# Optimization experiments

Hardware: AMD Instinct MI355X
Metric: run time of the kernel (lower is better)

The kernel has to match this reference:

```python
import jax, jax.numpy as jnp
import numpy as np

N = 50000          # num nodes
E = 1_600_000      # num edges (avg degree 32)
F = 512            # node_dim
C = 64             # num_clusters
O = 256            # output_dim


def setup_inputs() -> dict:
    key = jax.random.key(0)
    ks = jax.random.split(key, 9)
    lim_p = 1.0 / np.sqrt(F)
    inp = {
        "x": jax.random.normal(ks[0], (N, F), dtype=jnp.float32),
        "edge_index": jax.random.randint(ks[1], (2, E), 0, N, dtype=jnp.int64),
        "batch": jnp.zeros((N,), dtype=jnp.int64),
        # gnn_pool: Linear(F, C)
        "Wp": jax.random.uniform(ks[2], (F, C), jnp.float32, -lim_p, lim_p),
        "bp": jax.random.uniform(ks[3], (C,), jnp.float32, -lim_p, lim_p),
        # gnn_embed: Linear(F, F)
        "We": jax.random.uniform(ks[4], (F, F), jnp.float32, -lim_p, lim_p),
        "be": jax.random.uniform(ks[5], (F,), jnp.float32, -lim_p, lim_p),
        # projection: Linear(F, O)
        "Wo": jax.random.uniform(ks[6], (F, O), jnp.float32, -lim_p, lim_p),
        "bo": jax.random.uniform(ks[7], (O,), jnp.float32, -lim_p, lim_p),
    }
    return inp


def reference(x, edge_index, batch, Wp, bp, We, be, Wo, bo):
    # s = softmax(gnn_pool(x), -1): soft cluster assignments  [N, C]
    s = jax.nn.softmax(x @ Wp + bp, axis=-1)
    # h = gnn_embed(x)  [N, F]
    h = x @ We + be
    # dense_diff_pool pooled features: out = s^T h  -> [C, F]
    # (out_adj = s^T A s and the link/entropy reg are computed by the
    #  original but discarded; they do not affect the returned output.)
    pooled = jnp.einsum("nc,nf->cf", s, h)
    # PyG dense_diff_pool unsqueezes 2D inputs to batch dim 1 -> [1, C, F]
    out = pooled[None] @ Wo + bo  # [1, C, O]
    return out
```

## Files before the change

kernel.cpp:

```cpp
#include <hip/hip_runtime.h>
#include <hip/hip_bf16.h>

typedef __attribute__((ext_vector_type(8))) short short8;
typedef __attribute__((ext_vector_type(4))) float floatx4;
typedef __attribute__((ext_vector_type(4))) unsigned uint4v;

#define FDIM 512
#define CDIM 64
#define ODIM 256
#define XSS 520
#define STS 72
#define XSW(r, f) ((f) ^ ((((r) >> 3) & 3) << 4))

__device__ __forceinline__ ushort f2bf(float f) {
    union { float f; unsigned u; } v; v.f = f;
    unsigned r = v.u + 0x7FFFu + ((v.u >> 16) & 1u);
    return (ushort)(r >> 16);
}
__device__ __forceinline__ float bf2f(unsigned hi16) {
    union { unsigned u; float f; } v; v.u = hi16 << 16; return v.f;
}

__global__ __launch_bounds__(256) void kWpT(const float* __restrict__ Wp,
                                            ushort* __restrict__ WpT) {
    int g = blockIdx.x * 256 + threadIdx.x;
    int f = g >> 6, c = g & 63;
    WpT[c * FDIM + f] = f2bf(Wp[f * CDIM + c]);
}

__global__ __launch_bounds__(512, 2) void kFused(
        const float* __restrict__ x, const ushort* __restrict__ WpT,
        const float* __restrict__ bp, ushort* __restrict__ part,
        float* __restrict__ cpart, int N, int nTiles, int P) {
    __shared__ ushort xs[64][XSS];
    __shared__ ushort sT[64][STS];
    __shared__ float red1[64][4];
    __shared__ float red2[64][4];

    const int t    = threadIdx.x;
    const int w    = t >> 6;
    const int lane = t & 63;
    const int l16  = lane & 15;
    const int q    = lane >> 4;
    const int ci   = w & 3;
    const int rg   = w >> 2;

    floatx4 acc[4][4];
#pragma unroll
    for (int mt = 0; mt < 4; ++mt)
#pragma unroll
        for (int nt = 0; nt < 4; ++nt) acc[mt][nt] = (floatx4){0.f, 0.f, 0.f, 0.f};
    float csp[4] = {0.f, 0.f, 0.f, 0.f};

    float bpv[4];
#pragma unroll
    for (int reg = 0; reg < 4; ++reg) bpv[reg] = bp[16 * ci + 4 * q + reg];

    const ushort* wb = WpT + (size_t)(16 * ci + l16) * FDIM + q * 8;
    const int permA0 = (((l16 >> 3) & 1)) << 4;
    const int permA1 = ((2 + ((l16 >> 3) & 1)) & 3) << 4;

    for (int tile = blockIdx.x; tile < nTiles; tile += P) {
        __syncthreads();
        const int row0 = tile * 64;

#pragma unroll
        for (int half = 0; half < 2; ++half) {
            floatx4 vv[8];
#pragma unroll
            for (int j = 0; j < 8; ++j) {
                int v = (half * 8 + j) * 512 + t;
                int r = v >> 7;
                int f4 = (v & 127) << 2;
                vv[j] = (floatx4){0.f, 0.f, 0.f, 0.f};
                if (row0 + r < N)
                    vv[j] = *(const floatx4*)(x + (size_t)(row0 + r) * FDIM + f4);
            }
#pragma unroll
            for (int j = 0; j < 8; ++j) {
                int v = (half * 8 + j) * 512 + t;
                int r = v >> 7;
                int f4 = (v & 127) << 2;
                uint2 pk;
                pk.x = (unsigned)f2bf(vv[j][0]) | ((unsigned)f2bf(vv[j][1]) << 16);
                pk.y = (unsigned)f2bf(vv[j][2]) | ((unsigned)f2bf(vv[j][3]) << 16);
                *(uint2*)&xs[r][XSW(r, f4)] = pk;
            }
        }
        __syncthreads();

        floatx4 acc1[2];
        acc1[0] = (floatx4){0.f, 0.f, 0.f, 0.f};
        acc1[1] = (floatx4){0.f, 0.f, 0.f, 0.f};
        const int r0p = 16 * (2 * rg) + l16;
        const int r1p = 16 * (2 * rg + 1) + l16;
#pragma unroll
        for (int kb = 0; kb < 4; ++kb) {
            short8 af[4];
#pragma unroll
            for (int ki = 0; ki < 4; ++ki)
                af[ki] = *(const short8*)(wb + kb * 128 + ki * 32);
#pragma unroll
            for (int ki = 0; ki < 4; ++ki) {
                const int cb = kb * 128 + ki * 32 + q * 8;
                short8 b0 = *(const short8*)&xs[r0p][cb ^ permA0];
                acc1[0] = __builtin_amdgcn_mfma_f32_16x16x32_bf16(af[ki], b0, acc1[0], 0, 0, 0);
                short8 b1 = *(const short8*)&xs[r1p][cb ^ permA1];
                acc1[1] = __builtin_amdgcn_mfma_f32_16x16x32_bf16(af[ki], b1, acc1[1], 0, 0, 0);
            }
        }

        float lg[2][4], rmax[2], rsi[2];
#pragma unroll
        for (int rt = 0; rt < 2; ++rt) {
#pragma unroll
            for (int reg = 0; reg < 4; ++reg) lg[rt][reg] = acc1[rt][reg] + bpv[reg];
            float m = fmaxf(fmaxf(lg[rt][0], lg[rt][1]), fmaxf(lg[rt][2], lg[rt][3]));
            m = fmaxf(m, __shfl_xor(m, 16));
            m = fmaxf(m, __shfl_xor(m, 32));
            if (lane < 16) red1[16 * (2 * rg + rt) + lane][ci] = m;
        }
        __syncthreads();
#pragma unroll
        for (int rt = 0; rt < 2; ++rt) {
            const int row = 16 * (2 * rg + rt) + l16;
            rmax[rt] = fmaxf(fmaxf(red1[row][0], red1[row][1]),
                             fmaxf(red1[row][2], red1[row][3]));
        }
#pragma unroll
        for (int rt = 0; rt < 2; ++rt) {
            float p = 0.f;
#pragma unroll
            for (int reg = 0; reg < 4; ++reg) {
                float e = __expf(lg[rt][reg] - rmax[rt]);
                lg[rt][reg] = e; p += e;
            }
            p += __shfl_xor(p, 16);
            p += __shfl_xor(p, 32);
            if (lane < 16) red2[16 * (2 * rg + rt) + lane][ci] = p;
        }
        __syncthreads();
#pragma unroll
        for (int rt = 0; rt < 2; ++rt) {
            const int row = 16 * (2 * rg + rt) + l16;
            rsi[rt] = 1.0f / (red2[row][0] + red2[row][1] +
                              red2[row][2] + red2[row][3]);
        }
#pragma unroll
        for (int rt = 0; rt < 2; ++rt) {
            const int row = 16 * (2 * rg + rt) + l16;
            bool valid = (row0 + row) < N;
#pragma unroll
            for (int reg = 0; reg < 4; ++reg) {
                float s = valid ? lg[rt][reg] * rsi[rt] : 0.f;
                sT[16 * ci + 4 * q + reg][row] = f2bf(s);
                csp[reg] += s;
            }
        }
        __syncthreads();

        short8 as_[2][4];
#pragma unroll
        for (int ks = 0; ks < 2; ++ks)
#pragma unroll
            for (int mt = 0; mt < 4; ++mt)
                as_[ks][mt] = *(const short8*)&sT[16 * mt + l16][ks * 32 + q * 8];
#pragma unroll
        for (int nt = 0; nt < 4; ++nt) {
            const int fcol = (64 * w + 16 * nt + l16) ^ (q << 4);
            short8 b0, b1;
#pragma unroll
            for (int j = 0; j < 8; ++j) {
                b0[j] = (short)xs[q * 8 + j][fcol];
                b1[j] = (short)xs[32 + q * 8 + j][fcol];
            }
#pragma unroll
            for (int mt = 0; mt < 4; ++mt) {
                acc[mt][nt] = __builtin_amdgcn_mfma_f32_16x16x32_bf16(
                    as_[0][mt], b0, acc[mt][nt], 0, 0, 0);
                acc[mt][nt] = __builtin_amdgcn_mfma_f32_16x16x32_bf16(
                    as_[1][mt], b1, acc[mt][nt], 0, 0, 0);
            }
        }
    }

#pragma unroll
    for (int reg = 0; reg < 4; ++reg) {
        float v = csp[reg];
        v += __shfl_xor(v, 1); v += __shfl_xor(v, 2);
        v += __shfl_xor(v, 4); v += __shfl_xor(v, 8);
        if (l16 == 0) red1[16 * ci + 4 * q + reg][rg] = v;
    }
    __syncthreads();
    if (t < 64) cpart[(size_t)blockIdx.x * CDIM + t] = red1[t][0] + red1[t][1];

    ushort* xf = &xs[0][0];
#pragma unroll
    for (int mt = 0; mt < 4; ++mt)
#pragma unroll
        for (int nt = 0; nt < 4; ++nt)
#pragma unroll
            for (int reg = 0; reg < 4; ++reg)
                xf[(16 * mt + 4 * q + reg) * FDIM + 64 * w + 16 * nt + l16] =
                    f2bf(acc[mt][nt][reg]);
    __syncthreads();
    const uint4v* src = (const uint4v*)xf;
    uint4v* dst = (uint4v*)(part + (size_t)blockIdx.x * (CDIM * FDIM));
#pragma unroll
    for (int i = 0; i < 8; ++i)
        dst[i * 512 + t] = src[i * 512 + t];
}

__global__ __launch_bounds__(512) void kR(const ushort* __restrict__ part,
                                          const float* __restrict__ cpart,
                                          float* __restrict__ colsum,
                                          float* __restrict__ Mp,
                                          int P, int pch) {
    __shared__ float ws8[8];
    const int c = blockIdx.x, pc = blockIdx.y, t = threadIdx.x;
    const int p0 = pc * pch, p1 = min(p0 + pch, P);

    float sum = 0.f;
    const ushort* pp = part + (size_t)c * FDIM + t;
#pragma unroll 4
    for (int p = p0; p < p1; ++p)
        sum += bf2f((unsigned)pp[(size_t)p * (CDIM * FDIM)]);
    Mp[((size_t)pc * CDIM + c) * FDIM + t] = sum;

    float cv = 0.f;
    {
        int p = p0 + t;
        if (p < p1) cv = cpart[(size_t)p * CDIM + c];
    }
    cv += __shfl_xor(cv, 1);  cv += __shfl_xor(cv, 2);
    cv += __shfl_xor(cv, 4);  cv += __shfl_xor(cv, 8);
    cv += __shfl_xor(cv, 16); cv += __shfl_xor(cv, 32);
    if ((t & 63) == 0) ws8[t >> 6] = cv;
    __syncthreads();
    if (t == 0) {
        float tot = 0.f;
#pragma unroll
        for (int i = 0; i < 8; ++i) tot += ws8[i];
        atomicAdd(colsum + c, tot);
    }
}

__global__ __launch_bounds__(512) void kC(const float* __restrict__ Mp,
                                          const float* __restrict__ colsum,
                                          const float* __restrict__ We,
                                          const float* __restrict__ be,
                                          const float* __restrict__ Wo,
                                          const float* __restrict__ bo,
                                          float* __restrict__ out) {
    __shared__ float Mrow[512];
    __shared__ float pooled[512];
    __shared__ float halves[2][256];
    const int c = blockIdx.x, t = threadIdx.x;

    float sum = 0.f;
#pragma unroll
    for (int pc = 0; pc < 8; ++pc)
        sum += Mp[((size_t)pc * CDIM + c) * FDIM + t];
    Mrow[t] = sum;
    __syncthreads();

    float a = colsum[c] * be[t];
#pragma unroll 16
    for (int k = 0; k < FDIM; ++k)
        a = fmaf(Mrow[k], We[(size_t)k * FDIM + t], a);
    pooled[t] = a;
    __syncthreads();

    const int o = t & 255, h = t >> 8;
    float b = 0.f;
#pragma unroll 16
    for (int kk = 0; kk < 256; ++kk) {
        int k = h * 256 + kk;
        b = fmaf(pooled[k], Wo[(size_t)k * ODIM + o], b);
    }
    halves[h][o] = b;
    __syncthreads();
    if (t < 256)
        out[(size_t)c * ODIM + t] = halves[0][t] + halves[1][t] + bo[t];
}

extern "C" void kernel_launch(void* const* d_in, const int* in_sizes, int n_in,
                              void* d_out, int out_size, void* d_ws, size_t ws_size,
                              hipStream_t stream) {
    const float* x  = (const float*)d_in[0];
    const float* Wp = (const float*)d_in[3];
    const float* bp = (const float*)d_in[4];
    const float* We = (const float*)d_in[5];
    const float* be = (const float*)d_in[6];
    const float* Wo = (const float*)d_in[7];
    const float* bo = (const float*)d_in[8];
    float* out = (float*)d_out;

    const int N = in_sizes[0] / FDIM;
    const int nTiles = (N + 63) / 64;

    char*   wsb    = (char*)d_ws;
    ushort* WpT    = (ushort*)wsb;
    float*  colsum = (float*)(wsb + 65536);
    float*  cpart  = (float*)(wsb + 66560);
    float*  Mp     = (float*)(wsb + 266752);
    const size_t PART_OFF = 1315328;
    ushort* part   = (ushort*)(wsb + PART_OFF);

    size_t avail = (ws_size > PART_OFF + 65536) ? (ws_size - PART_OFF) / 65536 : 1;
    int P = (int)(avail < (size_t)nTiles ? avail : (size_t)nTiles);
    if (P < 1) P = 1;
    const int pch = (P + 7) / 8;

    hipMemsetAsync(colsum, 0, 256, stream);
    kWpT<<<128, 256, 0, stream>>>(Wp, WpT);
    kFused<<<P, 512, 0, stream>>>(x, WpT, bp, part, cpart, N, nTiles, P);
    kR<<<dim3(CDIM, 8), 512, 0, stream>>>(part, cpart, colsum, Mp, P, pch);
    kC<<<CDIM, 512, 0, stream>>>(Mp, colsum, We, be, Wo, bo, out);
}
```

Before: 257.6 us.

## Stream x tiles into LDS via global_load_lds, halve tile rows, cap grid

Changes the x staging from register loads plus bf16 conversion into swizzled LDS to direct global-to-LDS DMA of fp32 rows, with conversion to bf16 done at MFMA operand read time. The row tile shrinks from 64 to 32 so the fp32 tile fits, and occupancy is raised to 4 blocks per CU. The grid is capped at 512 persistent blocks rather than one per tile, which reduces partial-result traffic in the reduction stage. In exchange, each tile pays extra per-element conversion work in both GEMMs, does more loop iterations with their barriers, and reads column-strided fp32 from LDS without swizzling.

```diff
diff --git a/kernel.cpp b/kernel.cpp
--- a/kernel.cpp
+++ b/kernel.cpp
@@ -8,9 +8,10 @@
 #define FDIM 512
 #define CDIM 64
 #define ODIM 256
-#define XSS 520
-#define STS 72
-#define XSW(r, f) ((f) ^ ((((r) >> 3) & 3) << 4))
+#define TR   32
+#define XSF  516
+#define STS 40
+#define MAXP 512
 
 __device__ __forceinline__ ushort f2bf(float f) {
     union { float f; unsigned u; } v; v.f = f;
@@ -19,6 +20,13 @@
 }
 __device__ __forceinline__ float bf2f(unsigned hi16) {
     union { unsigned u; float f; } v; v.u = hi16 << 16; return v.f;
+}
+
+__device__ __forceinline__ void gld16(const float* g, float* lds_base) {
+    __builtin_amdgcn_global_load_lds(
+        (const __attribute__((address_space(1))) unsigned int*)(const void*)g,
+        (__attribute__((address_space(3))) unsigned int*)(void*)lds_base,
+        16, 0, 0);
 }
 
 __global__ __launch_bounds__(256) void kWpT(const float* __restrict__ Wp,
@@ -28,14 +36,15 @@
     WpT[c * FDIM + f] = f2bf(Wp[f * CDIM + c]);
 }
 
-__global__ __launch_bounds__(512, 2) void kFused(
+__global__ __launch_bounds__(512, 4) void kFused(
         const float* __restrict__ x, const ushort* __restrict__ WpT,
         const float* __restrict__ bp, ushort* __restrict__ part,
         float* __restrict__ cpart, int N, int nTiles, int P) {
-    __shared__ ushort xs[64][XSS];
-    __shared__ ushort sT[64][STS];
-    __shared__ float red1[64][4];
-    __shared__ float red2[64][4];
+    __shared__ float  xsf[TR * XSF];
+    __shared__ ushort sT[CDIM][STS];
+    __shared__ float  red1[TR][4];
+    __shared__ float  red2[TR][4];
+    __shared__ float  cred[CDIM][2];
 
     const int t    = threadIdx.x;
     const int w    = t >> 6;
@@ -57,43 +66,28 @@
     for (int reg = 0; reg < 4; ++reg) bpv[reg] = bp[16 * ci + 4 * q + reg];
 
     const ushort* wb = WpT + (size_t)(16 * ci + l16) * FDIM + q * 8;
-    const int permA0 = (((l16 >> 3) & 1)) << 4;
-    const int permA1 = ((2 + ((l16 >> 3) & 1)) & 3) << 4;
 
     for (int tile = blockIdx.x; tile < nTiles; tile += P) {
         __syncthreads();
-        const int row0 = tile * 64;
-
-#pragma unroll
-        for (int half = 0; half < 2; ++half) {
-            floatx4 vv[8];
-#pragma unroll
-            for (int j = 0; j < 8; ++j) {
-                int v = (half * 8 + j) * 512 + t;
-                int r = v >> 7;
-                int f4 = (v & 127) << 2;
-                vv[j] = (floatx4){0.f, 0.f, 0.f, 0.f};
-                if (row0 + r < N)
-                    vv[j] = *(const floatx4*)(x + (size_t)(row0 + r) * FDIM + f4);
+        const int row0 = tile * TR;
+
+#pragma unroll
+        for (int i = 0; i < 8; ++i) {
+            const int c0 = w * 8 + i;
+            const int r  = c0 >> 1;
+            const int h  = c0 & 1;
+            float* lb = xsf + r * XSF + h * 256;
+            if (row0 + r < N) {
+                const float* g = x + (size_t)(row0 + r) * FDIM + h * 256 + lane * 4;
+                gld16(g, lb);
+            } else {
+                *(floatx4*)(lb + lane * 4) = (floatx4){0.f, 0.f, 0.f, 0.f};
             }
-#pragma unroll
-            for (int j = 0; j < 8; ++j) {
-                int v = (half * 8 + j) * 512 + t;
-                int r = v >> 7;
-                int f4 = (v & 127) << 2;
-                uint2 pk;
-                pk.x = (unsigned)f2bf(vv[j][0]) | ((unsigned)f2bf(vv[j][1]) << 16);
-                pk.y = (unsigned)f2bf(vv[j][2]) | ((unsigned)f2bf(vv[j][3]) << 16);
-                *(uint2*)&xs[r][XSW(r, f4)] = pk;
-            }
-        }
-        __syncthreads();
-
-        floatx4 acc1[2];
-        acc1[0] = (floatx4){0.f, 0.f, 0.f, 0.f};
-        acc1[1] = (floatx4){0.f, 0.f, 0.f, 0.f};
-        const int r0p = 16 * (2 * rg) + l16;
-        const int r1p = 16 * (2 * rg + 1) + l16;
+        }
+        __syncthreads();
+
+        floatx4 acc1 = (floatx4){0.f, 0.f, 0.f, 0.f};
+        const float* xr = xsf + (16 * rg + l16) * XSF;
 #pragma unroll
         for (int kb = 0; kb < 4; ++kb) {
             short8 af[4];
@@ -102,85 +96,65 @@
                 af[ki] = *(const short8*)(wb + kb * 128 + ki * 32);
 #pragma unroll
             for (int ki = 0; ki < 4; ++ki) {
-                const int cb = kb * 128 + ki * 32 + q * 8;
-                short8 b0 = *(const short8*)&xs[r0p][cb ^ permA0];
-                acc1[0] = __builtin_amdgcn_mfma_f32_16x16x32_bf16(af[ki], b0, acc1[0], 0, 0, 0);
-                short8 b1 = *(const short8*)&xs[r1p][cb ^ permA1];
-                acc1[1] = __builtin_amdgcn_mfma_f32_16x16x32_bf16(af[ki], b1, acc1[1], 0, 0, 0);
+                const int off = kb * 128 + ki * 32 + q * 8;
+                floatx4 u0 = *(const floatx4*)(xr + off);
+                floatx4 u1 = *(const floatx4*)(xr + off + 4);
+                short8 b;
+                b[0] = (short)f2bf(u0[0]); b[1] = (short)f2bf(u0[1]);
+                b[2] = (short)f2bf(u0[2]); b[3] = (short)f2bf(u0[3]);
+                b[4] = (short)f2bf(u1[0]); b[5] = (short)f2bf(u1[1]);
+                b[6] = (short)f2bf(u1[2]); b[7] = (short)f2bf(u1[3]);
+                acc1 = __builtin_amdgcn_mfma_f32_16x16x32_bf16(af[ki], b, acc1, 0, 0, 0);
             }
         }
 
-        float lg[2][4], rmax[2], rsi[2];
-#pragma unroll
-        for (int rt = 0; rt < 2; ++rt) {
-#pragma unroll
-            for (int reg = 0; reg < 4; ++reg) lg[rt][reg] = acc1[rt][reg] + bpv[reg];
-            float m = fmaxf(fmaxf(lg[rt][0], lg[rt][1]), fmaxf(lg[rt][2], lg[rt][3]));
-            m = fmaxf(m, __shfl_xor(m, 16));
-            m = fmaxf(m, __shfl_xor(m, 32));
-            if (lane < 16) red1[16 * (2 * rg + rt) + lane][ci] = m;
-        }
-        __syncthreads();
-#pragma unroll
-        for (int rt = 0; rt < 2; ++rt) {
-            const int row = 16 * (2 * rg + rt) + l16;
-            rmax[rt] = fmaxf(fmaxf(red1[row][0], red1[row][1]),
-                             fmaxf(red1[row][2], red1[row][3]));
-        }
-#pragma unroll
-        for (int rt = 0; rt < 2; ++rt) {
-            float p = 0.f;
-#pragma unroll
-            for (int reg = 0; reg < 4; ++reg) {
-                float e = __expf(lg[rt][reg] - rmax[rt]);
-                lg[rt][reg] = e; p += e;
-            }
-            p += __shfl_xor(p, 16);
-            p += __shfl_xor(p, 32);
-            if (lane < 16) red2[16 * (2 * rg + rt) + lane][ci] = p;
-        }
-        __syncthreads();
-#pragma unroll
-        for (int rt = 0; rt < 2; ++rt) {
-            const int row = 16 * (2 * rg + rt) + l16;
-            rsi[rt] = 1.0f / (red2[row][0] + red2[row][1] +
-                              red2[row][2] + red2[row][3]);
-        }
-#pragma unroll
-        for (int rt = 0; rt < 2; ++rt) {
-            const int row = 16 * (2 * rg + rt) + l16;
-            bool valid = (row0 + row) < N;
-#pragma unroll
-            for (int reg = 0; reg < 4; ++reg) {
-                float s = valid ? lg[rt][reg] * rsi[rt] : 0.f;
-                sT[16 * ci + 4 * q + reg][row] = f2bf(s);
-                csp[reg] += s;
-            }
-        }
-        __syncthreads();
-
-        short8 as_[2][4];
-#pragma unroll
-        for (int ks = 0; ks < 2; ++ks)
+        const int row = 16 * rg + l16;
+        float lg[4];
+#pragma unroll
+        for (int reg = 0; reg < 4; ++reg) lg[reg] = acc1[reg] + bpv[reg];
+        float m = fmaxf(fmaxf(lg[0], lg[1]), fmaxf(lg[2], lg[3]));
+        m = fmaxf(m, __shfl_xor(m, 16));
+        m = fmaxf(m, __shfl_xor(m, 32));
+        if (lane < 16) red1[16 * rg + lane][ci] = m;
+        __syncthreads();
+        const float rmax = fmaxf(fmaxf(red1[row][0], red1[row][1]),
+                                 fmaxf(red1[row][2], red1[row][3]));
+        float p = 0.f;
+#pragma unroll
+        for (int reg = 0; reg < 4; ++reg) {
+            float e = __expf(lg[reg] - rmax);
+            lg[reg] = e; p += e;
+        }
+        p += __shfl_xor(p, 16);
+        p += __shfl_xor(p, 32);
+        if (lane < 16) red2[16 * rg + lane][ci] = p;
+        __syncthreads();
+        const float rsi = 1.0f / (red2[row][0] + red2[row][1] +
+                                  red2[row][2] + red2[row][3]);
+        const bool valid = (row0 + row) < N;
+#pragma unroll
+        for (int reg = 0; reg < 4; ++reg) {
+            float s = valid ? lg[reg] * rsi : 0.f;
+            sT[16 * ci + 4 * q + reg][row] = f2bf(s);
+            csp[reg] += s;
+        }
+        __syncthreads();
+
+        short8 as_[4];
+#pragma unroll
+        for (int mt = 0; mt < 4; ++mt)
+            as_[mt] = *(const short8*)&sT[16 * mt + l16][q * 8];
+#pragma unroll
+        for (int nt = 0; nt < 4; ++nt) {
+            const int f = 64 * w + 16 * nt + l16;
+            short8 b;
+#pragma unroll
+            for (int j = 0; j < 8; ++j)
+                b[j] = (short)f2bf(xsf[(q * 8 + j) * XSF + f]);
 #pragma unroll
             for (int mt = 0; mt < 4; ++mt)
-                as_[ks][mt] = *(const short8*)&sT[16 * mt + l16][ks * 32 + q * 8];
-#pragma unroll
-        for (int nt = 0; nt < 4; ++nt) {
-            const int fcol = (64 * w + 16 * nt + l16) ^ (q << 4);
-            short8 b0, b1;
-#pragma unroll
-            for (int j = 0; j < 8; ++j) {
-                b0[j] = (short)xs[q * 8 + j][fcol];
-                b1[j] = (short)xs[32 + q * 8 + j][fcol];
-            }
-#pragma unroll
-            for (int mt = 0; mt < 4; ++mt) {
                 acc[mt][nt] = __builtin_amdgcn_mfma_f32_16x16x32_bf16(
-                    as_[0][mt], b0, acc[mt][nt], 0, 0, 0);
-                acc[mt][nt] = __builtin_amdgcn_mfma_f32_16x16x32_bf16(
-                    as_[1][mt], b1, acc[mt][nt], 0, 0, 0);
-            }
+                    as_[mt], b, acc[mt][nt], 0, 0, 0);
         }
     }
 
@@ -189,12 +163,12 @@
         float v = csp[reg];
         v += __shfl_xor(v, 1); v += __shfl_xor(v, 2);
         v += __shfl_xor(v, 4); v += __shfl_xor(v, 8);
-        if (l16 == 0) red1[16 * ci + 4 * q + reg][rg] = v;
-    }
-    __syncthreads();
-    if (t < 64) cpart[(size_t)blockIdx.x * CDIM + t] = red1[t][0] + red1[t][1];
-
-    ushort* xf = &xs[0][0];
+        if (l16 == 0) cred[16 * ci + 4 * q + reg][rg] = v;
+    }
+    __syncthreads();
+    if (t < 64) cpart[(size_t)blockIdx.x * CDIM + t] = cred[t][0] + cred[t][1];
+
+    ushort* xf = (ushort*)xsf;
 #pragma unroll
     for (int mt = 0; mt < 4; ++mt)
 #pragma unroll
@@ -297,7 +271,7 @@
     float* out = (float*)d_out;
 
     const int N = in_sizes[0] / FDIM;
-    const int nTiles = (N + 63) / 64;
+    const int nTiles = (N + TR - 1) / TR;
 
     char*   wsb    = (char*)d_ws;
     ushort* WpT    = (ushort*)wsb;
@@ -308,7 +282,8 @@
     ushort* part   = (ushort*)(wsb + PART_OFF);
 
     size_t avail = (ws_size > PART_OFF + 65536) ? (ws_size - PART_OFF) / 65536 : 1;
-    int P = (int)(avail < (size_t)nTiles ? avail : (size_t)nTiles);
+    int P = (int)(avail < (size_t)MAXP ? avail : (size_t)MAXP);
+    if (P > nTiles) P = nTiles;
     if (P < 1) P = 1;
     const int pch = (P + 7) / 8;
 
```

Result: slower. 283.6 us (+10.1%).
